# Kernel tuning notes

Hardware: AMD Instinct MI355X
Metric: run time of the kernel (lower is better)

Reference implementation:

```python
import jax, jax.numpy as jnp
import numpy as np

F_SIZE = 1024
N_HEADS = 16
HEAD = F_SIZE // N_HEADS
EPS = 1e-5


def setup_inputs() -> dict:
    key = jax.random.key(0)
    ks = jax.random.split(key, 8)
    B, N, F = 4, 1024, F_SIZE
    in_feats = jax.random.normal(ks[0], (B, N, F), dtype=jnp.float32)
    pos_feats = jax.random.normal(ks[1], (B, N, F), dtype=jnp.float32)
    # parameters (torch Linear convention: W [out, in], y = x @ W.T + b)
    xav = lambda k, o, i: jax.random.uniform(k, (o, i), jnp.float32, -1.0, 1.0) * np.sqrt(6.0 / (o + i))
    ln_g = jnp.ones((F,), jnp.float32)
    ln_b = jnp.zeros((F,), jnp.float32)
    w_qk = xav(ks[2], 2 * F, F)
    b_qk = jnp.zeros((2 * F,), jnp.float32)
    w_v = xav(ks[3], F, F)
    b_v = jnp.zeros((F,), jnp.float32)
    w_o = xav(ks[4], F, F)
    b_o = jnp.zeros((F,), jnp.float32)
    return {"in_feats": in_feats, "pos_feats": pos_feats, "ln_g": ln_g, "ln_b": ln_b,
            "w_qk": w_qk, "b_qk": b_qk, "w_v": w_v, "b_v": b_v, "w_o": w_o, "b_o": b_o}


def reference(in_feats, pos_feats, ln_g, ln_b, w_qk, b_qk, w_v, b_v, w_o, b_o):
    B, N, F = in_feats.shape
    H, D = N_HEADS, HEAD
    # LayerNorm (biased variance, eps=1e-5 as torch default)
    mu = jnp.mean(in_feats, axis=-1, keepdims=True)
    var = jnp.mean(jnp.square(in_feats - mu), axis=-1, keepdims=True)
    norm = (in_feats - mu) * jax.lax.rsqrt(var + EPS) * ln_g + ln_b
    pos_norm = norm + pos_feats
    # QK projection on pos-added features, V projection on norm features
    qk = pos_norm @ w_qk.T + b_qk                      # [B,N,2F]
    q = qk[..., :F].reshape(B, N, H, D)
    k = qk[..., F:].reshape(B, N, H, D)
    v = (norm @ w_v.T + b_v).reshape(B, N, H, D)
    scale = float(D) ** -0.5
    scores = jnp.einsum('bnhd,bmhd->bhnm', q, k) * scale
    attn = jax.nn.softmax(scores, axis=-1)
    wv = jnp.einsum('bhnm,bmhd->bnhd', attn, v).reshape(B, N, F)
    delta = wv @ w_o.T + b_o
    return in_feats + delta
```

## Files before the change

kernel.cpp:

```cpp
#include <hip/hip_runtime.h>
#include <hip/hip_bf16.h>
#include <stdint.h>

#define FDIM 1024
#define NHEADS 16
#define HDIM 64
#define BATCH 4
#define SEQ 1024
#define MROWS (BATCH*SEQ)

typedef short bf16x8 __attribute__((ext_vector_type(8)));
typedef float f32x4 __attribute__((ext_vector_type(4)));

__device__ inline unsigned short f2bf(float f){
  union { float f; uint32_t u; } v; v.f = f;
  uint32_t u = v.u;
  uint32_t r = (u + 0x7fffu + ((u >> 16) & 1u)) >> 16;
  return (unsigned short)r;
}

__device__ inline void gld_lds16(const void* g, void* l){
  __builtin_amdgcn_global_load_lds((const __attribute__((address_space(1))) uint32_t*)g,
                                   (__attribute__((address_space(3))) uint32_t*)l, 16, 0, 0);
}

__device__ inline bf16x8 ldsw(const unsigned short* base, int row, int colgrp){
  return *(const bf16x8*)&base[row*64 + (((colgrp) ^ (row&7))<<3)];
}

__global__ __launch_bounds__(256) void cvt_w(const float* __restrict__ src,
                                             unsigned short* __restrict__ dst, int n4){
  int i = blockIdx.x*256 + threadIdx.x;
  if (i < n4){
    float4 v = ((const float4*)src)[i];
    ushort4 o; o.x=f2bf(v.x); o.y=f2bf(v.y); o.z=f2bf(v.z); o.w=f2bf(v.w);
    ((ushort4*)dst)[i] = o;
  }
}

__global__ __launch_bounds__(256) void ln_posadd(const float* __restrict__ x,
                                                 const float* __restrict__ pos,
                                                 const float* __restrict__ g,
                                                 const float* __restrict__ be,
                                                 unsigned short* __restrict__ normb,
                                                 unsigned short* __restrict__ posnb){
  int row = blockIdx.x, t = threadIdx.x;
  float4 v = ((const float4*)(x + (size_t)row*FDIM))[t];
  float s  = v.x+v.y+v.z+v.w;
  float sq = v.x*v.x+v.y*v.y+v.z*v.z+v.w*v.w;
  #pragma unroll
  for (int off=32; off>=1; off>>=1){ s += __shfl_down(s,off); sq += __shfl_down(sq,off); }
  __shared__ float red[8];
  int w=t>>6, lane=t&63;
  if (!lane){ red[w]=s; red[4+w]=sq; }
  __syncthreads();
  s  = red[0]+red[1]+red[2]+red[3];
  sq = red[4]+red[5]+red[6]+red[7];
  float mu  = s*(1.0f/FDIM);
  float var = sq*(1.0f/FDIM) - mu*mu;
  float rs  = rsqrtf(var + 1e-5f);
  float4 gg=((const float4*)g)[t], bb=((const float4*)be)[t];
  float4 pp=((const float4*)(pos + (size_t)row*FDIM))[t];
  float n0=(v.x-mu)*rs*gg.x+bb.x, n1=(v.y-mu)*rs*gg.y+bb.y;
  float n2=(v.z-mu)*rs*gg.z+bb.z, n3=(v.w-mu)*rs*gg.w+bb.w;
  ushort4 nb; nb.x=f2bf(n0); nb.y=f2bf(n1); nb.z=f2bf(n2); nb.w=f2bf(n3);
  ushort4 pb; pb.x=f2bf(n0+pp.x); pb.y=f2bf(n1+pp.y); pb.z=f2bf(n2+pp.z); pb.w=f2bf(n3+pp.w);
  ((ushort4*)(normb+(size_t)row*FDIM))[t]=nb;
  ((ushort4*)(posnb+(size_t)row*FDIM))[t]=pb;
}

template<int MODE>
__global__ __launch_bounds__(256) void gemm_bt(const unsigned short* __restrict__ A,
                                               const unsigned short* __restrict__ Bw,
                                               const float* __restrict__ bias,
                                               const float* __restrict__ resid,
                                               void* __restrict__ Cout,
                                               int M, int Nout, int K){
  __shared__ unsigned short Als[128*32];
  __shared__ unsigned short Bls[128*32];
  int t = threadIdx.x, w = t>>6, lane = t&63;
  int m0 = blockIdx.x*128, n0 = blockIdx.y*128;
  int wm = (w>>1)*64, wn = (w&1)*64;
  int lrow = lane&15, lk = (lane>>4)*8, rg = lane>>4;
  f32x4 acc[4][4] = {};
  for (int k0=0; k0<K; k0+=32){
    #pragma unroll
    for (int i=0;i<2;i++){
      int c = t + i*256;
      gld_lds16(A  + (size_t)(m0 + (c>>2))*K + k0 + (c&3)*8, Als + c*8);
      gld_lds16(Bw + (size_t)(n0 + (c>>2))*K + k0 + (c&3)*8, Bls + c*8);
    }
    __syncthreads();
    bf16x8 a[4], b[4];
    #pragma unroll
    for (int i=0;i<4;i++){
      a[i] = *(const bf16x8*)&Als[(wm + i*16 + lrow)*32 + lk];
      b[i] = *(const bf16x8*)&Bls[(wn + i*16 + lrow)*32 + lk];
    }
    #pragma unroll
    for (int mi=0;mi<4;mi++)
      #pragma unroll
      for (int ni=0;ni<4;ni++)
        acc[mi][ni] = __builtin_amdgcn_mfma_f32_16x16x32_bf16(a[mi], b[ni], acc[mi][ni], 0,0,0);
    __syncthreads();
  }
  #pragma unroll
  for (int mi=0;mi<4;mi++){
    #pragma unroll
    for (int ni=0;ni<4;ni++){
      int n = n0 + wn + ni*16 + lrow;
      float bs = bias[n];
      #pragma unroll
      for (int r=0;r<4;r++){
        int m = m0 + wm + mi*16 + rg*4 + r;
        float vv = acc[mi][ni][r] + bs;
        size_t idx = (size_t)m*Nout + n;
        if (MODE==0) ((unsigned short*)Cout)[idx] = f2bf(vv);
        else         ((float*)Cout)[idx] = vv + resid[idx];
      }
    }
  }
}

__global__ __launch_bounds__(256) void attn(const unsigned short* __restrict__ qk,
                                            const unsigned short* __restrict__ vbuf,
                                            unsigned short* __restrict__ wvbuf){
  __shared__ unsigned short Qls[64*64];
  __shared__ unsigned short Kls[64*64];
  __shared__ unsigned short Vtls[64*64];
  __shared__ unsigned short Pls[64*64];
  int t=threadIdx.x, w=t>>6, lane=t&63;
  int lrow=lane&15, lcg=lane>>4, rg=lane>>4;
  int bid = blockIdx.x;
  int wgid = (bid&7)*128 + (bid>>3);
  int q0 = (wgid&15)*64, h = (wgid>>4)&15, b = wgid>>8;
  const size_t qs = 2*FDIM;
  #pragma unroll
  for (int i=0;i<2;i++){
    int c=t+i*256, row=c>>3, cg=(c&7)^(row&7);
    gld_lds16(qk + (size_t)(b*SEQ + q0 + row)*qs + h*HDIM + cg*8, Qls + c*8);
  }
  f32x4 o[4] = {};
  float m_run[4], l_run[4];
  #pragma unroll
  for (int r=0;r<4;r++){ m_run[r]=-1e30f; l_run[r]=0.f; }
  __syncthreads();
  bf16x8 qa[2];
  qa[0] = ldsw(Qls, w*16+lrow, 0*4 + lcg);
  qa[1] = ldsw(Qls, w*16+lrow, 1*4 + lcg);

  const float SCL = 0.125f * 1.44269504f;

  for (int kt=0; kt<16; ++kt){
    int key0 = kt*64;
    __syncthreads();
    #pragma unroll
    for (int i=0;i<2;i++){
      int c=t+i*256, row=c>>3, cg=(c&7)^(row&7);
      gld_lds16(qk + (size_t)(b*SEQ + key0 + row)*qs + FDIM + h*HDIM + cg*8, Kls + c*8);
    }
    #pragma unroll
    for (int i=0;i<2;i++){
      int c=t+i*256;
      int key=c&63, d0=(c>>6)*8;
      bf16x8 vv = *(const bf16x8*)(vbuf + (size_t)(b*SEQ + key0 + key)*FDIM + h*HDIM + d0);
      #pragma unroll
      for (int j=0;j<8;j++)
        Vtls[(d0+j)*64 + ((((key>>3) ^ j))<<3) + (key&7)] = (unsigned short)vv[j];
    }
    __syncthreads();
    f32x4 s[4] = {};
    #pragma unroll
    for (int kf=0; kf<2; kf++){
      #pragma unroll
      for (int ni=0;ni<4;ni++){
        bf16x8 kb = ldsw(Kls, ni*16+lrow, kf*4 + lcg);
        s[ni] = __builtin_amdgcn_mfma_f32_16x16x32_bf16(qa[kf], kb, s[ni], 0,0,0);
      }
    }
    #pragma unroll
    for (int r=0;r<4;r++){
      float tm = fmaxf(fmaxf(s[0][r],s[1][r]), fmaxf(s[2][r],s[3][r])) * SCL;
      #pragma unroll
      for (int off=1; off<16; off<<=1) tm = fmaxf(tm, __shfl_xor(tm, off));
      float mn = fmaxf(m_run[r], tm);
      float sc = exp2f(m_run[r] - mn);
      float p[4]; float ts = 0.f;
      #pragma unroll
      for (int ni=0;ni<4;ni++){ p[ni] = exp2f(s[ni][r]*SCL - mn); ts += p[ni]; }
      #pragma unroll
      for (int off=1; off<16; off<<=1) ts += __shfl_xor(ts, off);
      l_run[r] = l_run[r]*sc + ts;
      m_run[r] = mn;
      #pragma unroll
      for (int nd=0;nd<4;nd++) o[nd][r] *= sc;
      int pr = w*16 + rg*4 + r;
      #pragma unroll
      for (int ni=0;ni<4;ni++)
        Pls[pr*64 + (((ni*2 + (lrow>>3)) ^ (pr&7))<<3) + (lrow&7)] = f2bf(p[ni]);
    }
    #pragma unroll
    for (int kf=0; kf<2; kf++){
      bf16x8 pa = ldsw(Pls, w*16+lrow, kf*4 + lcg);
      #pragma unroll
      for (int nd=0;nd<4;nd++){
        bf16x8 vb = ldsw(Vtls, nd*16+lrow, kf*4 + lcg);
        o[nd] = __builtin_amdgcn_mfma_f32_16x16x32_bf16(pa, vb, o[nd], 0,0,0);
      }
    }
  }
  #pragma unroll
  for (int nd=0; nd<4; nd++){
    #pragma unroll
    for (int r=0;r<4;r++){
      float val = o[nd][r] / l_run[r];
      wvbuf[(size_t)(b*SEQ + q0 + w*16 + rg*4 + r)*FDIM + h*HDIM + nd*16 + lrow] = f2bf(val);
    }
  }
}

extern "C" void kernel_launch(void* const* d_in, const int* in_sizes, int n_in,
                              void* d_out, int out_size, void* d_ws, size_t ws_size,
                              hipStream_t stream) {
  const float* in_feats = (const float*)d_in[0];
  const float* pos      = (const float*)d_in[1];
  const float* ln_g     = (const float*)d_in[2];
  const float* ln_b     = (const float*)d_in[3];
  const float* w_qk     = (const float*)d_in[4];
  const float* b_qk     = (const float*)d_in[5];
  const float* w_v      = (const float*)d_in[6];
  const float* b_v      = (const float*)d_in[7];
  const float* w_o      = (const float*)d_in[8];
  const float* b_o      = (const float*)d_in[9];
  float* out = (float*)d_out;

  char* ws = (char*)d_ws;
  unsigned short* norm_b = (unsigned short*)(ws + 0);
  unsigned short* posn_b = (unsigned short*)(ws + (8u<<20));
  unsigned short* wqk_b  = (unsigned short*)(ws + (16u<<20));
  unsigned short* wv_b   = (unsigned short*)(ws + (20u<<20));
  unsigned short* wo_b   = (unsigned short*)(ws + (22u<<20));
  unsigned short* qk_buf = (unsigned short*)(ws + (24u<<20));
  unsigned short* v_buf  = (unsigned short*)(ws + (40u<<20));
  unsigned short* wv_out = norm_b;

  cvt_w<<<(2048*1024/4 + 255)/256, 256, 0, stream>>>(w_qk, wqk_b, 2048*1024/4);
  cvt_w<<<(1024*1024/4 + 255)/256, 256, 0, stream>>>(w_v,  wv_b,  1024*1024/4);
  cvt_w<<<(1024*1024/4 + 255)/256, 256, 0, stream>>>(w_o,  wo_b,  1024*1024/4);
  ln_posadd<<<MROWS, 256, 0, stream>>>(in_feats, pos, ln_g, ln_b, norm_b, posn_b);
  gemm_bt<0><<<dim3(MROWS/128, 2048/128), 256, 0, stream>>>(posn_b, wqk_b, b_qk, nullptr,
                                                            qk_buf, MROWS, 2048, FDIM);
  gemm_bt<0><<<dim3(MROWS/128, 1024/128), 256, 0, stream>>>(norm_b, wv_b, b_v, nullptr,
                                                            v_buf, MROWS, 1024, FDIM);
  attn<<<dim3(SEQ/64 * NHEADS * BATCH), 256, 0, stream>>>(qk_buf, v_buf, wv_out);
  gemm_bt<1><<<dim3(MROWS/128, 1024/128), 256, 0, stream>>>(wv_out, wo_b, b_o, in_feats,
                                                            out, MROWS, 1024, FDIM);
}
```

Baseline: 268.8 us.

## Produce transposed V via GEMM, double-buffer K/V in attention, use DPP reductions

The V projection now computes V^T directly by swapping GEMM operands, with a new mode that applies bias per output row. This lets the attention kernel load V tiles with async global-to-LDS copies instead of transposing them through scalar LDS stores. The attention loop double-buffers K and V^T so the next tile's loads overlap the current tile's compute, and it drops one barrier per iteration. Row max and sum reductions use DPP row rotations instead of shuffles, and the three weight-conversion launches are merged into one. The cost is twice the K/V LDS footprint, which may lower occupancy.

Result: faster. 257.2 us (-4.3%).

```diff
diff --git a/kernel.cpp b/kernel.cpp
--- a/kernel.cpp
+++ b/kernel.cpp
@@ -28,14 +28,35 @@
   return *(const bf16x8*)&base[row*64 + (((colgrp) ^ (row&7))<<3)];
 }
 
-__global__ __launch_bounds__(256) void cvt_w(const float* __restrict__ src,
-                                             unsigned short* __restrict__ dst, int n4){
+template<int N>
+__device__ inline float dppRor(float x){
+  int r = __builtin_amdgcn_update_dpp(0, __float_as_int(x), 0x120|N, 0xF, 0xF, true);
+  return __int_as_float(r);
+}
+__device__ inline float rowMax16(float x){
+  x = fmaxf(x, dppRor<1>(x)); x = fmaxf(x, dppRor<2>(x));
+  x = fmaxf(x, dppRor<4>(x)); x = fmaxf(x, dppRor<8>(x));
+  return x;
+}
+__device__ inline float rowSum16(float x){
+  x += dppRor<1>(x); x += dppRor<2>(x); x += dppRor<4>(x); x += dppRor<8>(x);
+  return x;
+}
+
+__global__ __launch_bounds__(256) void cvt_all(const float* __restrict__ wqk,
+                                               const float* __restrict__ wv,
+                                               const float* __restrict__ wo,
+                                               unsigned short* __restrict__ oqk,
+                                               unsigned short* __restrict__ ov,
+                                               unsigned short* __restrict__ oo){
   int i = blockIdx.x*256 + threadIdx.x;
-  if (i < n4){
-    float4 v = ((const float4*)src)[i];
-    ushort4 o; o.x=f2bf(v.x); o.y=f2bf(v.y); o.z=f2bf(v.z); o.w=f2bf(v.w);
-    ((ushort4*)dst)[i] = o;
-  }
+  const float* src; unsigned short* dst; int j;
+  if (i < 524288)      { src = wqk; dst = oqk; j = i; }
+  else if (i < 786432) { src = wv;  dst = ov;  j = i - 524288; }
+  else                 { src = wo;  dst = oo;  j = i - 786432; }
+  float4 v = ((const float4*)src)[j];
+  ushort4 o; o.x=f2bf(v.x); o.y=f2bf(v.y); o.z=f2bf(v.z); o.w=f2bf(v.w);
+  ((ushort4*)dst)[j] = o;
 }
 
 __global__ __launch_bounds__(256) void ln_posadd(const float* __restrict__ x,
@@ -109,25 +130,25 @@
     #pragma unroll
     for (int ni=0;ni<4;ni++){
       int n = n0 + wn + ni*16 + lrow;
-      float bs = bias[n];
+      float bs = (MODE==2) ? 0.f : bias[n];
       #pragma unroll
       for (int r=0;r<4;r++){
         int m = m0 + wm + mi*16 + rg*4 + r;
-        float vv = acc[mi][ni][r] + bs;
+        float vv = acc[mi][ni][r] + ((MODE==2) ? bias[m] : bs);
         size_t idx = (size_t)m*Nout + n;
-        if (MODE==0) ((unsigned short*)Cout)[idx] = f2bf(vv);
-        else         ((float*)Cout)[idx] = vv + resid[idx];
+        if (MODE==1) ((float*)Cout)[idx] = vv + resid[idx];
+        else         ((unsigned short*)Cout)[idx] = f2bf(vv);
       }
     }
   }
 }
 
 __global__ __launch_bounds__(256) void attn(const unsigned short* __restrict__ qk,
-                                            const unsigned short* __restrict__ vbuf,
+                                            const unsigned short* __restrict__ vt,
                                             unsigned short* __restrict__ wvbuf){
   __shared__ unsigned short Qls[64*64];
-  __shared__ unsigned short Kls[64*64];
-  __shared__ unsigned short Vtls[64*64];
+  __shared__ unsigned short Kls[2][64*64];
+  __shared__ unsigned short Vtls[2][64*64];
   __shared__ unsigned short Pls[64*64];
   int t=threadIdx.x, w=t>>6, lane=t&63;
   int lrow=lane&15, lcg=lane>>4, rg=lane>>4;
@@ -135,10 +156,13 @@
   int wgid = (bid&7)*128 + (bid>>3);
   int q0 = (wgid&15)*64, h = (wgid>>4)&15, b = wgid>>8;
   const size_t qs = 2*FDIM;
+
   #pragma unroll
   for (int i=0;i<2;i++){
     int c=t+i*256, row=c>>3, cg=(c&7)^(row&7);
     gld_lds16(qk + (size_t)(b*SEQ + q0 + row)*qs + h*HDIM + cg*8, Qls + c*8);
+    gld_lds16(qk + (size_t)(b*SEQ + row)*qs + FDIM + h*HDIM + cg*8, Kls[0] + c*8);
+    gld_lds16(vt + (size_t)(h*HDIM + row)*MROWS + b*SEQ + cg*8, Vtls[0] + c*8);
   }
   f32x4 o[4] = {};
   float m_run[4], l_run[4];
@@ -150,46 +174,37 @@
   qa[1] = ldsw(Qls, w*16+lrow, 1*4 + lcg);
 
   const float SCL = 0.125f * 1.44269504f;
+  int cur = 0;
 
   for (int kt=0; kt<16; ++kt){
-    int key0 = kt*64;
-    __syncthreads();
-    #pragma unroll
-    for (int i=0;i<2;i++){
-      int c=t+i*256, row=c>>3, cg=(c&7)^(row&7);
-      gld_lds16(qk + (size_t)(b*SEQ + key0 + row)*qs + FDIM + h*HDIM + cg*8, Kls + c*8);
-    }
-    #pragma unroll
-    for (int i=0;i<2;i++){
-      int c=t+i*256;
-      int key=c&63, d0=(c>>6)*8;
-      bf16x8 vv = *(const bf16x8*)(vbuf + (size_t)(b*SEQ + key0 + key)*FDIM + h*HDIM + d0);
-      #pragma unroll
-      for (int j=0;j<8;j++)
-        Vtls[(d0+j)*64 + ((((key>>3) ^ j))<<3) + (key&7)] = (unsigned short)vv[j];
-    }
-    __syncthreads();
+    if (kt < 15){
+      int key1 = (kt+1)*64;
+      #pragma unroll
+      for (int i=0;i<2;i++){
+        int c=t+i*256, row=c>>3, cg=(c&7)^(row&7);
+        gld_lds16(qk + (size_t)(b*SEQ + key1 + row)*qs + FDIM + h*HDIM + cg*8, Kls[cur^1] + c*8);
+        gld_lds16(vt + (size_t)(h*HDIM + row)*MROWS + b*SEQ + key1 + cg*8, Vtls[cur^1] + c*8);
+      }
+    }
     f32x4 s[4] = {};
     #pragma unroll
     for (int kf=0; kf<2; kf++){
       #pragma unroll
       for (int ni=0;ni<4;ni++){
-        bf16x8 kb = ldsw(Kls, ni*16+lrow, kf*4 + lcg);
+        bf16x8 kb = ldsw(Kls[cur], ni*16+lrow, kf*4 + lcg);
         s[ni] = __builtin_amdgcn_mfma_f32_16x16x32_bf16(qa[kf], kb, s[ni], 0,0,0);
       }
     }
     #pragma unroll
     for (int r=0;r<4;r++){
       float tm = fmaxf(fmaxf(s[0][r],s[1][r]), fmaxf(s[2][r],s[3][r])) * SCL;
-      #pragma unroll
-      for (int off=1; off<16; off<<=1) tm = fmaxf(tm, __shfl_xor(tm, off));
+      tm = rowMax16(tm);
       float mn = fmaxf(m_run[r], tm);
       float sc = exp2f(m_run[r] - mn);
       float p[4]; float ts = 0.f;
       #pragma unroll
       for (int ni=0;ni<4;ni++){ p[ni] = exp2f(s[ni][r]*SCL - mn); ts += p[ni]; }
-      #pragma unroll
-      for (int off=1; off<16; off<<=1) ts += __shfl_xor(ts, off);
+      ts = rowSum16(ts);
       l_run[r] = l_run[r]*sc + ts;
       m_run[r] = mn;
       #pragma unroll
@@ -204,10 +219,12 @@
       bf16x8 pa = ldsw(Pls, w*16+lrow, kf*4 + lcg);
       #pragma unroll
       for (int nd=0;nd<4;nd++){
-        bf16x8 vb = ldsw(Vtls, nd*16+lrow, kf*4 + lcg);
+        bf16x8 vb = ldsw(Vtls[cur], nd*16+lrow, kf*4 + lcg);
         o[nd] = __builtin_amdgcn_mfma_f32_16x16x32_bf16(pa, vb, o[nd], 0,0,0);
       }
     }
+    __syncthreads();
+    cur ^= 1;
   }
   #pragma unroll
   for (int nd=0; nd<4; nd++){
@@ -241,18 +258,16 @@
   unsigned short* wv_b   = (unsigned short*)(ws + (20u<<20));
   unsigned short* wo_b   = (unsigned short*)(ws + (22u<<20));
   unsigned short* qk_buf = (unsigned short*)(ws + (24u<<20));
-  unsigned short* v_buf  = (unsigned short*)(ws + (40u<<20));
+  unsigned short* vt_buf = (unsigned short*)(ws + (40u<<20));
   unsigned short* wv_out = norm_b;
 
-  cvt_w<<<(2048*1024/4 + 255)/256, 256, 0, stream>>>(w_qk, wqk_b, 2048*1024/4);
-  cvt_w<<<(1024*1024/4 + 255)/256, 256, 0, stream>>>(w_v,  wv_b,  1024*1024/4);
-  cvt_w<<<(1024*1024/4 + 255)/256, 256, 0, stream>>>(w_o,  wo_b,  1024*1024/4);
+  cvt_all<<<4096, 256, 0, stream>>>(w_qk, w_v, w_o, wqk_b, wv_b, wo_b);
   ln_posadd<<<MROWS, 256, 0, stream>>>(in_feats, pos, ln_g, ln_b, norm_b, posn_b);
   gemm_bt<0><<<dim3(MROWS/128, 2048/128), 256, 0, stream>>>(posn_b, wqk_b, b_qk, nullptr,
                                                             qk_buf, MROWS, 2048, FDIM);
-  gemm_bt<0><<<dim3(MROWS/128, 1024/128), 256, 0, stream>>>(norm_b, wv_b, b_v, nullptr,
-                                                            v_buf, MROWS, 1024, FDIM);
-  attn<<<dim3(SEQ/64 * NHEADS * BATCH), 256, 0, stream>>>(qk_buf, v_buf, wv_out);
+  gemm_bt<2><<<dim3(FDIM/128, MROWS/128), 256, 0, stream>>>(wv_b, norm_b, b_v, nullptr,
+                                                            vt_buf, FDIM, MROWS, FDIM);
+  attn<<<dim3(SEQ/64 * NHEADS * BATCH), 256, 0, stream>>>(qk_buf, vt_buf, wv_out);
   gemm_bt<1><<<dim3(MROWS/128, 1024/128), 256, 0, stream>>>(wv_out, wo_b, b_o, in_feats,
                                                             out, MROWS, 1024, FDIM);
 }
```
